# Kernel tuning notes

Measured on AMD Instinct MI355X. Metric: run time of the kernel, lower is better.

Reference implementation:

```python
import jax, jax.numpy as jnp
import numpy as np

N, E, B = 4096, 4096, 128  # nodes, edges, graphs


def _param(key, shape, scale):
    return jax.random.normal(key, shape, dtype=jnp.float32) * scale


def setup_inputs() -> dict:
    key = jax.random.key(0)
    ks = jax.random.split(key, 32)
    inp = {
        "x": jax.random.normal(ks[0], (N, 37), dtype=jnp.float32),
        "edge_index": jax.random.randint(ks[1], (2, E), 0, N),
        "edge_attr": jax.random.uniform(ks[2], (E, 5), dtype=jnp.float32),
        "batch": jnp.sort(jax.random.randint(ks[3], (N,), 0, B)),
        # NNConv 1: edge-MLP 5->512->37*128, root [37,128]
        "nn1_w1": _param(ks[4], (5, 512), 0.3),
        "nn1_b1": jnp.zeros((512,), jnp.float32),
        "nn1_w2": _param(ks[5], (512, 37 * 128), 0.01),
        "nn1_b2": jnp.zeros((37 * 128,), jnp.float32),
        "root1": _param(ks[6], (37, 128), 0.1),
        "bias1": jnp.zeros((128,), jnp.float32),
        # NNConv 2: edge-MLP 5->128->128*256, root [128,256]
        "nn2_w1": _param(ks[7], (5, 128), 0.3),
        "nn2_b1": jnp.zeros((128,), jnp.float32),
        "nn2_w2": _param(ks[8], (128, 128 * 256), 0.005),
        "nn2_b2": jnp.zeros((128 * 256,), jnp.float32),
        "root2": _param(ks[9], (128, 256), 0.05),
        "bias2": jnp.zeros((256,), jnp.float32),
        # NNConv 3: edge-MLP 5->128->256*256, root [256,256]
        "nn3_w1": _param(ks[10], (5, 128), 0.3),
        "nn3_b1": jnp.zeros((128,), jnp.float32),
        "nn3_w2": _param(ks[11], (128, 256 * 256), 0.005),
        "nn3_b2": jnp.zeros((256 * 256,), jnp.float32),
        "root3": _param(ks[12], (256, 256), 0.05),
        "bias3": jnp.zeros((256,), jnp.float32),
        # readout MLP
        "fc1_w": _param(ks[13], (256, 128), 0.06),
        "fc1_b": jnp.zeros((128,), jnp.float32),
        "fc2_w": _param(ks[14], (128, 64), 0.09),
        "fc2_b": jnp.zeros((64,), jnp.float32),
        "fc3_w": _param(ks[15], (64, 1), 0.12),
        "fc3_b": jnp.zeros((1,), jnp.float32),
    }
    return inp


def _nnconv(x, src, dst, edge_attr, w1, b1, w2, b2, root, bias, cin, cout):
    # edge MLP -> per-edge weight matrix [E, cin, cout]
    h = jax.nn.relu(edge_attr @ w1 + b1)
    W = (h @ w2 + b2).reshape(-1, cin, cout)
    # gather source features, per-edge matvec, scatter-add to targets
    msg = jnp.einsum('ei,eio->eo', x[src], W)          # [E, cout]
    agg = jax.ops.segment_sum(msg, dst, num_segments=x.shape[0])
    return agg + x @ root + bias


def _segment_mean(x, seg, num_segments):
    s = jax.ops.segment_sum(x, seg, num_segments=num_segments)
    cnt = jax.ops.segment_sum(jnp.ones((x.shape[0],), x.dtype), seg,
                              num_segments=num_segments)
    return s / jnp.maximum(cnt, 1.0)[:, None]


def reference(x, edge_index, edge_attr, batch,
              nn1_w1, nn1_b1, nn1_w2, nn1_b2, root1, bias1,
              nn2_w1, nn2_b1, nn2_w2, nn2_b2, root2, bias2,
              nn3_w1, nn3_b1, nn3_w2, nn3_b2, root3, bias3,
              fc1_w, fc1_b, fc2_w, fc2_b, fc3_w, fc3_b):
    src, dst = edge_index[0], edge_index[1]
    h = jax.nn.elu(_nnconv(x, src, dst, edge_attr, nn1_w1, nn1_b1, nn1_w2,
                           nn1_b2, root1, bias1, 37, 128))
    h = jax.nn.elu(_nnconv(h, src, dst, edge_attr, nn2_w1, nn2_b1, nn2_w2,
                           nn2_b2, root2, bias2, 128, 256))
    h = jax.nn.elu(_nnconv(h, src, dst, edge_attr, nn3_w1, nn3_b1, nn3_w2,
                           nn3_b2, root3, bias3, 256, 256))
    g = _segment_mean(h, batch, B)                     # [B, 256]
    g = jax.nn.elu(g @ fc1_w + fc1_b)
    g = jax.nn.elu(g @ fc2_w + fc2_b)
    g = g @ fc3_w + fc3_b
    return g.reshape(-1)
```

## Files before the change

### kernel.cpp

```cpp
#include <hip/hip_runtime.h>
#include <cstdint>
#include <cstddef>

typedef float f32x4 __attribute__((ext_vector_type(4)));
typedef _Float16 f16x8 __attribute__((ext_vector_type(8)));
typedef _Float16 f16x4 __attribute__((ext_vector_type(4)));

__device__ __forceinline__ float elu_f(float x) { return x > 0.f ? x : expm1f(x); }

template <int CIN, int COUT, int KFTOT>
__device__ __forceinline__
void pack_body(int bid, int tid, const float* __restrict__ w2, const float* __restrict__ b2,
               _Float16* __restrict__ w2h, int KH, float* tile )
{
    const int kh = bid / KFTOT;
    const int c  = bid - kh * KFTOT;
    const int CP = 32 * COUT;
    for (int i = tid; i < CP; i += 256) {
        int kk = i / COUT, n = i - kk * COUT;
        int kg = c * 32 + kk;
        float v = 0.f;
        if (kg < CIN) v = (kh < KH) ? w2[((size_t)kh * CIN + kg) * COUT + n]
                                    : b2[(size_t)kg * COUT + n];
        tile[kk * (COUT + 2) + n] = v;
    }
    __syncthreads();
    _Float16* outp = w2h + (size_t)bid * CP;
    for (int i = tid; i < CP; i += 256) {
        int n = i >> 5, kk = i & 31;
        outp[n * 32 + kk] = (_Float16)tile[kk * (COUT + 2) + n];
    }
}

__global__ __launch_bounds__(256)
void uber_prologue_kernel(const float* __restrict__ ea,
                          const int* __restrict__ dst, int* __restrict__ cnt,
                          const float* __restrict__ w1a, const float* __restrict__ b1a, _Float16* __restrict__ h1T,
                          const float* __restrict__ w1b, const float* __restrict__ b1b, _Float16* __restrict__ h2T,
                          const float* __restrict__ w1c, const float* __restrict__ b1c, _Float16* __restrict__ h3T,
                          int E,
                          const float* __restrict__ w2a, const float* __restrict__ b2a, _Float16* __restrict__ w2h1,
                          const float* __restrict__ w2b, const float* __restrict__ b2b, _Float16* __restrict__ w2h2,
                          const float* __restrict__ w2c, const float* __restrict__ b2c, _Float16* __restrict__ w2h3)
{
    __shared__ __align__(16) float smem[32 * 258];
    const int tid = threadIdx.x;
    const int nEB = E >> 6;
    int b = blockIdx.x;

    if (b < nEB) {
        const int e0 = b * 64;
        const int el = tid & 63;
        const int cg = tid >> 6;
        if (tid < 64) atomicAdd(&cnt[dst[e0 + tid]], 1);
        float* a = smem;
        for (int i = tid; i < 320; i += 256) a[(i / 5) * 5 + (i % 5)] = ea[e0 * 5 + i];
        __syncthreads();
        float av[5];
        #pragma unroll
        for (int j = 0; j < 5; ++j) av[j] = a[el * 5 + j];
        #pragma unroll 4
        for (int t = 0; t < 128; ++t) {
            const int ch = t * 4 + cg;
            float s = b1a[ch];
            #pragma unroll
            for (int j = 0; j < 5; ++j) s = fmaf(av[j], w1a[j * 512 + ch], s);
            h1T[(size_t)ch * E + e0 + el] = (_Float16)fmaxf(s, 0.f);
        }
        #pragma unroll 4
        for (int t = 0; t < 32; ++t) {
            const int ch = t * 4 + cg;
            float s = b1b[ch];
            float u = b1c[ch];
            #pragma unroll
            for (int j = 0; j < 5; ++j) {
                s = fmaf(av[j], w1b[j * 128 + ch], s);
                u = fmaf(av[j], w1c[j * 128 + ch], u);
            }
            h2T[(size_t)ch * E + e0 + el] = (_Float16)fmaxf(s, 0.f);
            h3T[(size_t)ch * E + e0 + el] = (_Float16)fmaxf(u, 0.f);
        }
        return;
    }
    b -= nEB;
    if (b < 513 * 2) { pack_body<37, 128, 2>(b, tid, w2a, b2a, w2h1, 512, smem); return; }
    b -= 513 * 2;
    if (b < 129 * 4) { pack_body<128, 256, 4>(b, tid, w2b, b2b, w2h2, 128, smem); return; }
    b -= 129 * 4;
    pack_body<256, 256, 8>(b, tid, w2c, b2c, w2h3, 128, smem);
}

__global__ __launch_bounds__(256)
void csr_scan_graph_kernel(const int* __restrict__ cnt, int* __restrict__ offs, int N,
                           const int* __restrict__ batch, int* __restrict__ goffs, int B,
                           int NN)
{
    __shared__ int sums[256];
    __shared__ int pref[257];
    const int tid = threadIdx.x;
    const int per = N / 256;
    int loc = 0;
    for (int i = 0; i < per; ++i) loc += cnt[tid * per + i];
    sums[tid] = loc;
    __syncthreads();
    if (tid == 0) {
        int s = 0; pref[0] = 0;
        for (int i = 0; i < 256; ++i) { s += sums[i]; pref[i + 1] = s; }
    }
    __syncthreads();
    int run = pref[tid];
    for (int i = 0; i < per; ++i) { offs[tid * per + i] = run; run += cnt[tid * per + i]; }
    if (tid == 255) offs[N] = run;
    for (int g = tid; g <= B; g += 256) {
        int lo = 0, hi = NN;
        while (lo < hi) { int mid = (lo + hi) >> 1; if (batch[mid] < g) lo = mid + 1; else hi = mid; }
        goffs[g] = lo;
    }
}

__global__ __launch_bounds__(256)
void csr_fill_kernel(const int* __restrict__ dst, const int* __restrict__ offs,
                     int* __restrict__ cur, int* __restrict__ eid, int E)
{
    int e = blockIdx.x * 256 + threadIdx.x;
    if (e < E) {
        int d = dst[e];
        int p = offs[d] + atomicAdd(&cur[d], 1);
        eid[p] = e;
    }
}

template <int KH, int CIN, int COUT, int KFTOT, int CSPLIT, int NY>
__global__ __launch_bounds__(256, 4)
void msg_mfma_kernel(const float* __restrict__ xin,
                     const _Float16* __restrict__ hT,
                     const _Float16* __restrict__ w2h,
                     const int* __restrict__ src,
                     _Float16* __restrict__ part,
                     int E, int khg_per)
{
    constexpr int BM = 256;
    constexpr int KF = KFTOT / CSPLIT;
    static_assert(KF == 1, "direct-L2 msg kernel expects one 32-k chunk per block");

    __shared__ int s_src[BM];

    const int tid  = threadIdx.x;
    const int lane = tid & 63;
    const int w    = tid >> 6;
    const int l15  = lane & 15;
    const int lg   = lane >> 4;

    const int nwg = gridDim.x;
    const int bid = blockIdx.x;
    const int swz = (bid & 7) * (nwg >> 3) + (bid >> 3);
    const int m    = swz & 15;
    const int rest = swz >> 4;
    const int y    = rest % NY;
    const int zz   = rest / NY;
    const int cinH = zz % CSPLIT;
    const int zkh  = zz / CSPLIT;

    const int e0  = m * BM;
    const int n0  = y * 64;
    const int k0  = cinH * 32;
    const int kh0 = zkh * khg_per;
    const int kh1 = min(kh0 + khg_per, KH + 1);

    s_src[tid] = src[e0 + tid];
    __syncthreads();

    f16x8 a_[4];
    #pragma unroll
    for (int mf = 0; mf < 4; ++mf) {
        const int eloc = w * 64 + mf * 16 + l15;
        const float* xrow = xin + (size_t)s_src[eloc] * CIN + k0;
        if (CIN % 32 == 0) {
            float4 p0 = *(const float4*)(xrow + lg * 8);
            float4 p1 = *(const float4*)(xrow + lg * 8 + 4);
            a_[mf][0] = (_Float16)p0.x; a_[mf][1] = (_Float16)p0.y;
            a_[mf][2] = (_Float16)p0.z; a_[mf][3] = (_Float16)p0.w;
            a_[mf][4] = (_Float16)p1.x; a_[mf][5] = (_Float16)p1.y;
            a_[mf][6] = (_Float16)p1.z; a_[mf][7] = (_Float16)p1.w;
        } else {
            #pragma unroll
            for (int j = 0; j < 8; ++j) {
                int kk = lg * 8 + j;
                float v = (k0 + kk < CIN) ? xrow[kk] : 0.f;
                a_[mf][j] = (_Float16)v;
            }
        }
    }

    f32x4 msg[4][4];
    #pragma unroll
    for (int mf = 0; mf < 4; ++mf)
        #pragma unroll
        for (int nf = 0; nf < 4; ++nf) msg[mf][nf] = 0.f;

    const int bro = l15 * 32 + lg * 8;

    for (int khg = kh0; khg < kh1; ++khg) {
        const _Float16* cb = w2h + ((size_t)(khg * KFTOT + cinH) * COUT + n0) * 32;

        f16x8 Bv[4];
        #pragma unroll
        for (int nf = 0; nf < 4; ++nf)
            Bv[nf] = *(const f16x8*)(cb + nf * 512 + bro);

        _Float16 hh[4];
        if (khg < KH) {
            const _Float16* hp = hT + (size_t)khg * E + e0 + w * 64 + l15;
            #pragma unroll
            for (int mf = 0; mf < 4; ++mf) hh[mf] = hp[mf * 16];
        } else {
            #pragma unroll
            for (int mf = 0; mf < 4; ++mf) hh[mf] = (_Float16)1.0f;
        }

        #pragma unroll
        for (int mf = 0; mf < 4; ++mf) {
            f16x8 ah = a_[mf] * hh[mf];
            #pragma unroll
            for (int nf = 0; nf < 4; ++nf)
                msg[mf][nf] = __builtin_amdgcn_mfma_f32_16x16x32_f16(ah, Bv[nf], msg[mf][nf], 0, 0, 0);
        }
    }

    _Float16* pb = part + ((size_t)zz * E + e0) * COUT + n0;
    #pragma unroll
    for (int mf = 0; mf < 4; ++mf)
        #pragma unroll
        for (int r = 0; r < 4; ++r) {
            const int row = w * 64 + mf * 16 + lg * 4 + r;
            #pragma unroll
            for (int nf = 0; nf < 4; ++nf)
                pb[(size_t)row * COUT + nf * 16 + l15] = (_Float16)msg[mf][nf][r];
        }
}

template <int CIN, int COUT, int Z>
__global__ __launch_bounds__(256)
void node_gemm_kernel(const float* __restrict__ xin,
                      const float* __restrict__ root,
                      const _Float16* __restrict__ part,
                      const int* __restrict__ offs,
                      const int* __restrict__ eid,
                      const float* __restrict__ bias,
                      float* __restrict__ out, int E)
{
    constexpr int BM  = 64;
    constexpr int BN  = 64;
    constexpr int BKI = (CIN % 32 == 0) ? 32 : 16;
    constexpr int CIN_PAD = ((CIN + BKI - 1) / BKI) * BKI;
    constexpr int CPK = CIN_PAD / BKI;
    constexpr int NROWS = BKI / 16;

    __shared__ __align__(16) float xs_t[CIN_PAD][BM];
    __shared__ __align__(16) float btile[BKI][BN];

    const int tid = threadIdx.x;
    const int tx  = tid & 15;
    const int ty  = tid >> 4;
    const int ty4 = ty * 4;
    const int tx4 = tx * 4;
    const int e0  = blockIdx.x * BM;
    const int n0  = blockIdx.y * BN;

    for (int idx = tid; idx < BM * CIN_PAD; idx += 256) {
        int mm = idx / CIN_PAD;
        int i  = idx - mm * CIN_PAD;
        float v = 0.f;
        if (i < CIN) v = xin[(size_t)(e0 + mm) * CIN + i];
        xs_t[i][mm] = v;
    }

    const int rbase = tid >> 4;
    const int nn    = (tid & 15) * 4;
    float acc[4][4] = {};
    float4 pre[NROWS];

    {
        const float* brow = root + n0;
        #pragma unroll
        for (int rr = 0; rr < NROWS; ++rr) {
            int r = rbase + rr * 16;
            float4 v = {0.f, 0.f, 0.f, 0.f};
            if (r < CIN) v = *(const float4*)(brow + (size_t)r * COUT + nn);
            pre[rr] = v;
        }
    }

    for (int c = 0; c < CPK; ++c) {
        __syncthreads();
        #pragma unroll
        for (int rr = 0; rr < NROWS; ++rr)
            *(float4*)&btile[rbase + rr * 16][nn] = pre[rr];
        __syncthreads();

        if (c + 1 < CPK) {
            int i0n = (c + 1) * BKI;
            const float* brow = root + (size_t)i0n * COUT + n0;
            #pragma unroll
            for (int rr = 0; rr < NROWS; ++rr) {
                int r = rbase + rr * 16;
                float4 v = {0.f, 0.f, 0.f, 0.f};
                if (i0n + r < CIN) v = *(const float4*)(brow + (size_t)r * COUT + nn);
                pre[rr] = v;
            }
        }

        const int i0 = c * BKI;
        #pragma unroll
        for (int ii = 0; ii < BKI; ++ii) {
            float4 xv = *(const float4*)&xs_t[i0 + ii][ty4];
            float4 bv = *(const float4*)&btile[ii][tx4];
            float av[4] = {xv.x, xv.y, xv.z, xv.w};
            float bvv[4] = {bv.x, bv.y, bv.z, bv.w};
            #pragma unroll
            for (int mm = 0; mm < 4; ++mm)
                #pragma unroll
                for (int nq = 0; nq < 4; ++nq)
                    acc[mm][nq] = fmaf(av[mm], bvv[nq], acc[mm][nq]);
        }
    }

    float bs[4];
    #pragma unroll
    for (int nq = 0; nq < 4; ++nq) bs[nq] = bias[n0 + tx4 + nq];

    #pragma unroll
    for (int mm = 0; mm < 4; ++mm) {
        const int row = e0 + ty4 + mm;
        float add[4] = {0.f, 0.f, 0.f, 0.f};
        const int b = offs[row], t = offs[row + 1];
        for (int j = b; j < t; ++j) {
            const int e = eid[j];
            #pragma unroll
            for (int z = 0; z < Z; ++z) {
                f16x4 r4 = *(const f16x4*)(part + ((size_t)z * E + e) * COUT + n0 + tx4);
                add[0] += (float)r4.x; add[1] += (float)r4.y;
                add[2] += (float)r4.z; add[3] += (float)r4.w;
            }
        }
        size_t base = (size_t)row * COUT + n0 + tx4;
        #pragma unroll
        for (int nq = 0; nq < 4; ++nq)
            out[base + nq] = elu_f(acc[mm][nq] + add[nq] + bs[nq]);
    }
}

__global__ __launch_bounds__(256)
void pool_readout_kernel(const float* __restrict__ hl3, const int* __restrict__ goffs,
                         const float* __restrict__ fc1w, const float* __restrict__ fc1b,
                         const float* __restrict__ fc2w, const float* __restrict__ fc2b,
                         const float* __restrict__ fc3w, const float* __restrict__ fc3b,
                         float* __restrict__ outp)
{
    const int g   = blockIdx.x;
    const int tid = threadIdx.x;
    __shared__ float gm[256];
    __shared__ float a1[128];
    __shared__ float a2[64];
    const int b = goffs[g], t = goffs[g + 1];
    float s = 0.f;
    for (int n = b; n < t; ++n) s += hl3[(size_t)n * 256 + tid];
    gm[tid] = s / fmaxf((float)(t - b), 1.f);
    __syncthreads();
    if (tid < 128) {
        float v = fc1b[tid];
        for (int j = 0; j < 256; ++j) v = fmaf(gm[j], fc1w[j * 128 + tid], v);
        a1[tid] = elu_f(v);
    }
    __syncthreads();
    if (tid < 64) {
        float v = fc2b[tid];
        for (int j = 0; j < 128; ++j) v = fmaf(a1[j], fc2w[j * 64 + tid], v);
        a2[tid] = elu_f(v);
    }
    __syncthreads();
    if (tid == 0) {
        float v = fc3b[0];
        for (int j = 0; j < 64; ++j) v = fmaf(a2[j], fc3w[j], v);
        outp[g] = v;
    }
}

extern "C" void kernel_launch(void* const* d_in, const int* in_sizes, int n_in,
                              void* d_out, int out_size, void* d_ws, size_t ws_size,
                              hipStream_t stream)
{
    const float* x      = (const float*)d_in[0];
    const int*   ei     = (const int*)  d_in[1];
    const float* ea     = (const float*)d_in[2];
    const int*   batch  = (const int*)  d_in[3];
    const float* nn1_w1 = (const float*)d_in[4];
    const float* nn1_b1 = (const float*)d_in[5];
    const float* nn1_w2 = (const float*)d_in[6];
    const float* nn1_b2 = (const float*)d_in[7];
    const float* root1  = (const float*)d_in[8];
    const float* bias1  = (const float*)d_in[9];
    const float* nn2_w1 = (const float*)d_in[10];
    const float* nn2_b1 = (const float*)d_in[11];
    const float* nn2_w2 = (const float*)d_in[12];
    const float* nn2_b2 = (const float*)d_in[13];
    const float* root2  = (const float*)d_in[14];
    const float* bias2  = (const float*)d_in[15];
    const float* nn3_w1 = (const float*)d_in[16];
    const float* nn3_b1 = (const float*)d_in[17];
    const float* nn3_w2 = (const float*)d_in[18];
    const float* nn3_b2 = (const float*)d_in[19];
    const float* root3  = (const float*)d_in[20];
    const float* bias3  = (const float*)d_in[21];
    const float* fc1_w  = (const float*)d_in[22];
    const float* fc1_b  = (const float*)d_in[23];
    const float* fc2_w  = (const float*)d_in[24];
    const float* fc2_b  = (const float*)d_in[25];
    const float* fc3_w  = (const float*)d_in[26];
    const float* fc3_b  = (const float*)d_in[27];

    const int E = in_sizes[2] / 5;
    const int N = in_sizes[0] / 37;
    const int B = out_size;
    const int* srcp = ei;
    const int* dstp = ei + E;

    const size_t W1H = (size_t)513 * 2 * 128 * 32;
    const size_t W2H = (size_t)129 * 4 * 256 * 32;
    const size_t W3H = (size_t)129 * 8 * 256 * 32;
    _Float16* w2h1 = (_Float16*)d_ws;
    _Float16* w2h2 = w2h1 + W1H;
    _Float16* w2h3 = w2h2 + W2H;
    _Float16* h1T  = w2h3 + W3H;
    _Float16* h2T  = h1T + (size_t)512 * E;
    _Float16* h3T  = h2T + (size_t)128 * E;
    _Float16* part = h3T + (size_t)128 * E;
    float* fbase = (float*)(part + (size_t)32 * E * 128);
    float* hl1   = fbase;
    float* hl2   = hl1 + (size_t)N * 128;
    float* hl3   = hl2 + (size_t)N * 256;
    int* ibase   = (int*)(hl3 + (size_t)N * 256);
    int* cnt   = ibase;
    int* cur   = cnt + N;
    int* offs  = cur + N;
    int* eid   = offs + N + 1;
    int* goffs = eid + E;

    hipMemsetAsync(cnt, 0, 2 * N * sizeof(int), stream);

    const int nEB = E / 64;
    uber_prologue_kernel<<<nEB + 1026 + 516 + 1032, 256, 0, stream>>>(
        ea, dstp, cnt,
        nn1_w1, nn1_b1, h1T, nn2_w1, nn2_b1, h2T, nn3_w1, nn3_b1, h3T, E,
        nn1_w2, nn1_b2, w2h1, nn2_w2, nn2_b2, w2h2, nn3_w2, nn3_b2, w2h3);

    csr_scan_graph_kernel<<<1, 256, 0, stream>>>(cnt, offs, N, batch, goffs, B, N);
    csr_fill_kernel<<<(E + 255) / 256, 256, 0, stream>>>(dstp, offs, cur, eid, E);

    msg_mfma_kernel<512, 37, 128, 2, 2, 2><<<1024, 256, 0, stream>>>(
        x, h1T, w2h1, srcp, part, E, 33);
    node_gemm_kernel<37, 128, 32><<<dim3(N / 64, 2), 256, 0, stream>>>(
        x, root1, part, offs, eid, bias1, hl1, E);

    msg_mfma_kernel<128, 128, 256, 4, 4, 4><<<1024, 256, 0, stream>>>(
        hl1, h2T, w2h2, srcp, part, E, 33);
    node_gemm_kernel<128, 256, 16><<<dim3(N / 64, 4), 256, 0, stream>>>(
        hl1, root2, part, offs, eid, bias2, hl2, E);

    msg_mfma_kernel<128, 256, 256, 8, 8, 4><<<1024, 256, 0, stream>>>(
        hl2, h3T, w2h3, srcp, part, E, 65);
    node_gemm_kernel<256, 256, 16><<<dim3(N / 64, 4), 256, 0, stream>>>(
        hl2, root3, part, offs, eid, bias3, hl3, E);

    pool_readout_kernel<<<B, 256, 0, stream>>>(hl3, goffs, fc1_w, fc1_b,
                                               fc2_w, fc2_b, fc3_w, fc3_b,
                                               (float*)d_out);
}
```

Baseline: 324.5 us.

## Stage weight chunks via async global-to-LDS with double buffering and 512-edge tiles

```diff
diff --git a/kernel.cpp b/kernel.cpp
--- a/kernel.cpp
+++ b/kernel.cpp
@@ -7,6 +7,14 @@
 typedef _Float16 f16x4 __attribute__((ext_vector_type(4)));
 
 __device__ __forceinline__ float elu_f(float x) { return x > 0.f ? x : expm1f(x); }
+
+__device__ __forceinline__ void gload_lds16(const void* g, void* l)
+{
+    __builtin_amdgcn_global_load_lds(
+        (const __attribute__((address_space(1))) void*)g,
+        (__attribute__((address_space(3))) void*)l,
+        16, 0, 0);
+}
 
 template <int CIN, int COUT, int KFTOT>
 __device__ __forceinline__
@@ -28,7 +36,8 @@
     _Float16* outp = w2h + (size_t)bid * CP;
     for (int i = tid; i < CP; i += 256) {
         int n = i >> 5, kk = i & 31;
-        outp[n * 32 + kk] = (_Float16)tile[kk * (COUT + 2) + n];
+        int blk = (kk >> 3) ^ ((n >> 1) & 3);
+        outp[n * 32 + blk * 8 + (kk & 7)] = (_Float16)tile[kk * (COUT + 2) + n];
     }
 }
 
@@ -131,7 +140,7 @@
 }
 
 template <int KH, int CIN, int COUT, int KFTOT, int CSPLIT, int NY>
-__global__ __launch_bounds__(256, 4)
+__global__ __launch_bounds__(256, 2)
 void msg_mfma_kernel(const float* __restrict__ xin,
                      const _Float16* __restrict__ hT,
                      const _Float16* __restrict__ w2h,
@@ -139,10 +148,11 @@
                      _Float16* __restrict__ part,
                      int E, int khg_per)
 {
-    constexpr int BM = 256;
+    constexpr int BM = 512;
     constexpr int KF = KFTOT / CSPLIT;
-    static_assert(KF == 1, "direct-L2 msg kernel expects one 32-k chunk per block");
-
+    static_assert(KF == 1, "mf=8 msg kernel expects one 32-k chunk per block");
+
+    __shared__ __align__(16) _Float16 bsh[2][64][32];
     __shared__ int s_src[BM];
 
     const int tid  = threadIdx.x;
@@ -150,12 +160,13 @@
     const int w    = tid >> 6;
     const int l15  = lane & 15;
     const int lg   = lane >> 4;
+    const int swb  = (l15 >> 1) & 3;
 
     const int nwg = gridDim.x;
     const int bid = blockIdx.x;
     const int swz = (bid & 7) * (nwg >> 3) + (bid >> 3);
-    const int m    = swz & 15;
-    const int rest = swz >> 4;
+    const int m    = swz & 7;
+    const int rest = swz >> 3;
     const int y    = rest % NY;
     const int zz   = rest / NY;
     const int cinH = zz % CSPLIT;
@@ -167,13 +178,14 @@
     const int kh0 = zkh * khg_per;
     const int kh1 = min(kh0 + khg_per, KH + 1);
 
-    s_src[tid] = src[e0 + tid];
-    __syncthreads();
-
-    f16x8 a_[4];
+    s_src[tid]       = src[e0 + tid];
+    s_src[tid + 256] = src[e0 + tid + 256];
+    __syncthreads();
+
+    f16x8 a_[8];
     #pragma unroll
-    for (int mf = 0; mf < 4; ++mf) {
-        const int eloc = w * 64 + mf * 16 + l15;
+    for (int mf = 0; mf < 8; ++mf) {
+        const int eloc = w * 128 + mf * 16 + l15;
         const float* xrow = xin + (size_t)s_src[eloc] * CIN + k0;
         if (CIN % 32 == 0) {
             float4 p0 = *(const float4*)(xrow + lg * 8);
@@ -192,47 +204,59 @@
         }
     }
 
-    f32x4 msg[4][4];
+    f32x4 msg[8][4];
     #pragma unroll
-    for (int mf = 0; mf < 4; ++mf)
+    for (int mf = 0; mf < 8; ++mf)
         #pragma unroll
         for (int nf = 0; nf < 4; ++nf) msg[mf][nf] = 0.f;
 
-    const int bro = l15 * 32 + lg * 8;
-
+    auto stage = [&](int khg, int pp) {
+        if (khg >= kh1) return;
+        const size_t chunk = (size_t)khg * KFTOT + cinH;
+        const char* g = (const char*)(w2h + (chunk * COUT + n0) * 32) + (size_t)tid * 16;
+        char* l = (char*)(&bsh[pp][0][0]) + (tid >> 6) * 1024;
+        gload_lds16(g, l);
+    };
+
+    stage(kh0, 0);
+
+    int p = 0;
     for (int khg = kh0; khg < kh1; ++khg) {
-        const _Float16* cb = w2h + ((size_t)(khg * KFTOT + cinH) * COUT + n0) * 32;
+        __syncthreads();
+
+        stage(khg + 1, p ^ 1);
+
+        _Float16 hh[8];
+        if (khg < KH) {
+            const _Float16* hp = hT + (size_t)khg * E + e0 + w * 128 + l15;
+            #pragma unroll
+            for (int mf = 0; mf < 8; ++mf) hh[mf] = hp[mf * 16];
+        } else {
+            #pragma unroll
+            for (int mf = 0; mf < 8; ++mf) hh[mf] = (_Float16)1.0f;
+        }
 
         f16x8 Bv[4];
         #pragma unroll
         for (int nf = 0; nf < 4; ++nf)
-            Bv[nf] = *(const f16x8*)(cb + nf * 512 + bro);
-
-        _Float16 hh[4];
-        if (khg < KH) {
-            const _Float16* hp = hT + (size_t)khg * E + e0 + w * 64 + l15;
-            #pragma unroll
-            for (int mf = 0; mf < 4; ++mf) hh[mf] = hp[mf * 16];
-        } else {
-            #pragma unroll
-            for (int mf = 0; mf < 4; ++mf) hh[mf] = (_Float16)1.0f;
-        }
-
-        #pragma unroll
-        for (int mf = 0; mf < 4; ++mf) {
+            Bv[nf] = *(const f16x8*)&bsh[p][nf * 16 + l15][(lg ^ swb) * 8];
+
+        #pragma unroll
+        for (int mf = 0; mf < 8; ++mf) {
             f16x8 ah = a_[mf] * hh[mf];
             #pragma unroll
             for (int nf = 0; nf < 4; ++nf)
                 msg[mf][nf] = __builtin_amdgcn_mfma_f32_16x16x32_f16(ah, Bv[nf], msg[mf][nf], 0, 0, 0);
         }
+        p ^= 1;
     }
 
     _Float16* pb = part + ((size_t)zz * E + e0) * COUT + n0;
     #pragma unroll
-    for (int mf = 0; mf < 4; ++mf)
+    for (int mf = 0; mf < 8; ++mf)
         #pragma unroll
         for (int r = 0; r < 4; ++r) {
-            const int row = w * 64 + mf * 16 + lg * 4 + r;
+            const int row = w * 128 + mf * 16 + lg * 4 + r;
             #pragma unroll
             for (int nf = 0; nf < 4; ++nf)
                 pb[(size_t)row * COUT + nf * 16 + l15] = (_Float16)msg[mf][nf][r];
@@ -457,17 +481,17 @@
     csr_scan_graph_kernel<<<1, 256, 0, stream>>>(cnt, offs, N, batch, goffs, B, N);
     csr_fill_kernel<<<(E + 255) / 256, 256, 0, stream>>>(dstp, offs, cur, eid, E);
 
-    msg_mfma_kernel<512, 37, 128, 2, 2, 2><<<1024, 256, 0, stream>>>(
+    msg_mfma_kernel<512, 37, 128, 2, 2, 2><<<512, 256, 0, stream>>>(
         x, h1T, w2h1, srcp, part, E, 33);
     node_gemm_kernel<37, 128, 32><<<dim3(N / 64, 2), 256, 0, stream>>>(
         x, root1, part, offs, eid, bias1, hl1, E);
 
-    msg_mfma_kernel<128, 128, 256, 4, 4, 4><<<1024, 256, 0, stream>>>(
+    msg_mfma_kernel<128, 128, 256, 4, 4, 4><<<512, 256, 0, stream>>>(
         hl1, h2T, w2h2, srcp, part, E, 33);
     node_gemm_kernel<128, 256, 16><<<dim3(N / 64, 4), 256, 0, stream>>>(
         hl1, root2, part, offs, eid, bias2, hl2, E);
 
-    msg_mfma_kernel<128, 256, 256, 8, 8, 4><<<1024, 256, 0, stream>>>(
+    msg_mfma_kernel<128, 256, 256, 8, 8, 4><<<512, 256, 0, stream>>>(
         hl2, h3T, w2h3, srcp, part, E, 65);
     node_gemm_kernel<256, 256, 16><<<dim3(N / 64, 4), 256, 0, stream>>>(
         hl2, root3, part, offs, eid, bias3, hl3, E);
```

Result: faster. 297.8 us (-8.2%).
